# Optimization experiments

Hardware: AMD Instinct MI355X
Metric: run time of the kernel (lower is better)

## Reference

```python
import jax, jax.numpy as jnp
import numpy as np

N, IN, OUT, RANK = 8192, 4096, 4096, 256

def setup_inputs() -> dict:
    key = jax.random.key(0)
    ks = jax.random.split(key, 7)
    x = jax.random.normal(ks[0], (N, IN), dtype=jnp.float32)
    # original frozen linear layer params
    W = jax.random.normal(ks[1], (OUT, IN), dtype=jnp.float32) * (1.0 / np.sqrt(IN))
    bias = jax.random.normal(ks[2], (OUT,), dtype=jnp.float32) * 0.01
    # frozen shared low-rank matrices (kaiming-uniform-like scale)
    A_frozen = jax.random.normal(ks[3], (RANK, IN), dtype=jnp.float32) * (1.0 / np.sqrt(IN))
    B_frozen = jax.random.normal(ks[4], (OUT, RANK), dtype=jnp.float32) * (1.0 / np.sqrt(RANK))
    # trainable VeRA vectors (b_vec is zeros at init; use small randn so delta is nonzero)
    b_vec = jax.random.normal(ks[5], (OUT,), dtype=jnp.float32) * 0.01
    d_vec = jnp.full((RANK,), 0.1, dtype=jnp.float32) + jax.random.normal(ks[6], (RANK,), dtype=jnp.float32) * 0.01
    return {"x": x, "W": W, "bias": bias, "A_frozen": A_frozen, "B_frozen": B_frozen, "b_vec": b_vec, "d_vec": d_vec}

def reference(x, W, bias, A_frozen, B_frozen, b_vec, d_vec):
    # original frozen linear: [N, OUT]
    orig = x @ W.T + bias
    # diag(b) @ B @ diag(d) @ A @ x.T  ==  (((x @ A.T) * d) @ B.T) * b, transposed
    h = (x @ A_frozen.T) * d_vec            # [N, RANK]
    delta = (h @ B_frozen.T) * b_vec        # [N, OUT]
    return orig + delta
```

## Files before the change

kernel.cpp:

```cpp
#include <hip/hip_runtime.h>

#define IN_DIM 4096
#define OUT_DIM 4096
#define N_ROWS 8192
#define RANK 256

typedef __bf16 bf16x8 __attribute__((ext_vector_type(8)));
typedef float f32x4 __attribute__((ext_vector_type(4)));
typedef unsigned short u16;
typedef unsigned short u16x4 __attribute__((ext_vector_type(4)));

__device__ __forceinline__ u16 f2b(float f) {
    unsigned int u = __builtin_bit_cast(unsigned int, f);
    unsigned int r = u + 0x7FFFu + ((u >> 16) & 1u);
    return (u16)(r >> 16);
}

__device__ __forceinline__ void async16(const void* g, const void* l) {
    __builtin_amdgcn_global_load_lds(
        (const __attribute__((address_space(1))) void*)g,
        (__attribute__((address_space(3))) void*)l, 16, 0, 0);
}

__global__ __launch_bounds__(256) void cvt4(const float* __restrict__ s,
                                            u16* __restrict__ d, int n4) {
    int i = blockIdx.x * 256 + threadIdx.x;
    if (i >= n4) return;
    f32x4 v = __builtin_nontemporal_load((const f32x4*)s + i);
    u16x4 o;
    o.x = f2b(v.x); o.y = f2b(v.y); o.z = f2b(v.z); o.w = f2b(v.w);
    *((u16x4*)d + i) = o;
}

__global__ __launch_bounds__(256) void vera_adt(const float* __restrict__ A,
                                                const float* __restrict__ d,
                                                u16* __restrict__ adt) {
    int r = threadIdx.x;
    int i0 = blockIdx.x * 64;
    float dv = d[r];
    const float* ap = A + (size_t)r * IN_DIM + i0;
#pragma unroll 4
    for (int j = 0; j < 64; ++j)
        adt[(size_t)(i0 + j) * RANK + r] = f2b(__builtin_nontemporal_load(ap + j) * dv);
}

template <int MODE, int K, int NN, int TM, int TN>
__global__ __launch_bounds__(256) void vera_gemm(
    const u16* __restrict__ Aop, const u16* __restrict__ Bop,
    const float* __restrict__ W, const float* __restrict__ bvec,
    void* __restrict__ outv) {
    __shared__ __align__(16) __bf16 As[128 * 32];
    __shared__ __align__(16) __bf16 Bs[128 * 32];

    const int tid = threadIdx.x;
    const int lane = tid & 63;
    const int wavei = __builtin_amdgcn_readfirstlane(tid >> 6);
    const int fr = lane & 15;
    const int fq = lane >> 4;
    const int wm = (wavei >> 1) * 64;
    const int wn = (wavei & 1) * 64;

    constexpr int G = 8;
    const int bid = blockIdx.x;
    const int g = bid / (G * TN);
    const int r = bid - g * (G * TN);
    const int bm = (g * G + (r & (G - 1))) * 128;
    const int bn = (r / G) * 128;

    const int srow = tid >> 2;
    const int sk = (tid & 3) * 8;
    const u16* ga0 = Aop + (size_t)(bm + srow) * K + sk;
    const u16* ga1 = Aop + (size_t)(bm + 64 + srow) * K + sk;
    const u16* gb0 = Bop + (size_t)(bn + srow) * K + sk;
    const u16* gb1 = Bop + (size_t)(bn + 64 + srow) * K + sk;

    char* lAs = (char*)As;
    char* lBs = (char*)Bs;
    const int lo = wavei * 1024;

    f32x4 acc[4][4] = {};

    for (int k0 = 0; k0 < K; k0 += 32) {
        __syncthreads();
        async16(ga0 + k0, lAs + lo);
        async16(ga1 + k0, lAs + 4096 + lo);
        async16(gb0 + k0, lBs + lo);
        async16(gb1 + k0, lBs + 4096 + lo);
        __syncthreads();

        const __bf16* ap = As + (wm + fr) * 32 + fq * 8;
        const __bf16* bp = Bs + (wn + fr) * 32 + fq * 8;
        bf16x8 af[4], bfr[4];
#pragma unroll
        for (int i = 0; i < 4; ++i) {
            af[i] = *(const bf16x8*)(ap + i * 16 * 32);
            bfr[i] = *(const bf16x8*)(bp + i * 16 * 32);
        }
#pragma unroll
        for (int mi = 0; mi < 4; ++mi)
#pragma unroll
            for (int ni = 0; ni < 4; ++ni)
                acc[mi][ni] = __builtin_amdgcn_mfma_f32_16x16x32_bf16(
                    af[mi], bfr[ni], acc[mi][ni], 0, 0, 0);
    }

#pragma unroll
    for (int ni = 0; ni < 4; ++ni) {
        const int col = bn + wn + ni * 16 + fr;
        float bcol = (MODE == 1) ? bvec[col] : 0.f;
#pragma unroll
        for (int mi = 0; mi < 4; ++mi) {
            const int row0 = bm + wm + mi * 16 + fq * 4;
#pragma unroll
            for (int v = 0; v < 4; ++v) {
                const int row = row0 + v;
                float a = acc[mi][ni][v];
                if (MODE == 0) {
                    float wv = __builtin_nontemporal_load(&W[(size_t)row * NN + col]);
                    ((u16*)outv)[(size_t)row * NN + col] = f2b(wv + bvec[row] * a);
                } else {
                    __builtin_nontemporal_store(a + bcol,
                        &((float*)outv)[(size_t)row * NN + col]);
                }
            }
        }
    }
}

extern "C" void kernel_launch(void* const* d_in, const int* in_sizes, int n_in,
                              void* d_out, int out_size, void* d_ws, size_t ws_size,
                              hipStream_t stream) {
    (void)in_sizes; (void)n_in; (void)out_size; (void)ws_size;
    const float* x    = (const float*)d_in[0];
    const float* W    = (const float*)d_in[1];
    const float* bias = (const float*)d_in[2];
    const float* A    = (const float*)d_in[3];
    const float* B    = (const float*)d_in[4];
    const float* bv   = (const float*)d_in[5];
    const float* dv   = (const float*)d_in[6];

    char* ws = (char*)d_ws;
    u16* xb  = (u16*)ws;
    u16* wb  = (u16*)(ws + (size_t)N_ROWS * IN_DIM * 2);
    u16* adt = (u16*)(ws + (size_t)N_ROWS * IN_DIM * 2
                         + (size_t)OUT_DIM * IN_DIM * 2);
    u16* Bb  = adt + (size_t)IN_DIM * RANK;

    cvt4<<<dim3(OUT_DIM * RANK / 4 / 256), 256, 0, stream>>>(B, Bb, OUT_DIM * RANK / 4);
    vera_adt<<<dim3(IN_DIM / 64), 256, 0, stream>>>(A, dv, adt);
    vera_gemm<0, RANK, IN_DIM, OUT_DIM / 128, IN_DIM / 128>
        <<<dim3((OUT_DIM / 128) * (IN_DIM / 128)), 256, 0, stream>>>(
        Bb, adt, W, bv, wb);
    cvt4<<<dim3(N_ROWS * IN_DIM / 4 / 256), 256, 0, stream>>>(x, xb, N_ROWS * IN_DIM / 4);
    vera_gemm<1, IN_DIM, OUT_DIM, N_ROWS / 128, OUT_DIM / 128>
        <<<dim3((N_ROWS / 128) * (OUT_DIM / 128)), 256, 0, stream>>>(
        xb, wb, nullptr, bias, d_out);
}
```

Measured before the change: 608.9 us.

## Fuse prep kernels, overlap x conversion with weight GEMM, widen K step

Merges the B conversion and the A·diag(d) transpose into one prep kernel. The x fp32-to-bf16 conversion now runs in extra blocks appended to the weight-merging GEMM launch, so it overlaps with that GEMM. The main GEMM loads 64-wide K chunks per barrier pair instead of 32, which halves the number of sync rounds but doubles LDS use per block and may lower occupancy. Five launches become three.

```diff
diff --git a/kernel.cpp b/kernel.cpp
--- a/kernel.cpp
+++ b/kernel.cpp
@@ -22,37 +22,51 @@
         (__attribute__((address_space(3))) void*)l, 16, 0, 0);
 }
 
-__global__ __launch_bounds__(256) void cvt4(const float* __restrict__ s,
-                                            u16* __restrict__ d, int n4) {
-    int i = blockIdx.x * 256 + threadIdx.x;
-    if (i >= n4) return;
-    f32x4 v = __builtin_nontemporal_load((const f32x4*)s + i);
-    u16x4 o;
-    o.x = f2b(v.x); o.y = f2b(v.y); o.z = f2b(v.z); o.w = f2b(v.w);
-    *((u16x4*)d + i) = o;
+__global__ __launch_bounds__(256) void vera_prep(
+    const float* __restrict__ A, const float* __restrict__ dvec,
+    const float* __restrict__ B, u16* __restrict__ adt, u16* __restrict__ Bb) {
+    int b = blockIdx.x;
+    int t = threadIdx.x;
+    if (b < 128) {
+        int i0 = b * 32;
+        float dv = dvec[t];
+        const float* ap = A + (size_t)t * IN_DIM + i0;
+#pragma unroll 8
+        for (int j = 0; j < 32; ++j)
+            adt[(size_t)(i0 + j) * RANK + t] =
+                f2b(__builtin_nontemporal_load(ap + j) * dv);
+    } else {
+        int i = (b - 128) * 256 + t;
+        f32x4 v = __builtin_nontemporal_load((const f32x4*)B + i);
+        u16x4 o;
+        o.x = f2b(v.x); o.y = f2b(v.y); o.z = f2b(v.z); o.w = f2b(v.w);
+        *((u16x4*)Bb + i) = o;
+    }
 }
 
-__global__ __launch_bounds__(256) void vera_adt(const float* __restrict__ A,
-                                                const float* __restrict__ d,
-                                                u16* __restrict__ adt) {
-    int r = threadIdx.x;
-    int i0 = blockIdx.x * 64;
-    float dv = d[r];
-    const float* ap = A + (size_t)r * IN_DIM + i0;
-#pragma unroll 4
-    for (int j = 0; j < 64; ++j)
-        adt[(size_t)(i0 + j) * RANK + r] = f2b(__builtin_nontemporal_load(ap + j) * dv);
-}
-
-template <int MODE, int K, int NN, int TM, int TN>
+template <int MODE, int K, int NN, int TN, int GB>
 __global__ __launch_bounds__(256) void vera_gemm(
     const u16* __restrict__ Aop, const u16* __restrict__ Bop,
     const float* __restrict__ W, const float* __restrict__ bvec,
-    void* __restrict__ outv) {
-    __shared__ __align__(16) __bf16 As[128 * 32];
-    __shared__ __align__(16) __bf16 Bs[128 * 32];
+    void* __restrict__ outv,
+    const float* __restrict__ cvt_src, u16* __restrict__ cvt_dst, int cvt_n4) {
+    __shared__ __align__(16) __bf16 As[2 * 128 * 32];
+    __shared__ __align__(16) __bf16 Bs[2 * 128 * 32];
 
     const int tid = threadIdx.x;
+    const int bid = blockIdx.x;
+
+    if (bid >= GB) {
+        const int nb = gridDim.x - GB;
+        for (int i = (bid - GB) * 256 + tid; i < cvt_n4; i += nb * 256) {
+            f32x4 v = __builtin_nontemporal_load((const f32x4*)cvt_src + i);
+            u16x4 o;
+            o.x = f2b(v.x); o.y = f2b(v.y); o.z = f2b(v.z); o.w = f2b(v.w);
+            *((u16x4*)cvt_dst + i) = o;
+        }
+        return;
+    }
+
     const int lane = tid & 63;
     const int wavei = __builtin_amdgcn_readfirstlane(tid >> 6);
     const int fr = lane & 15;
@@ -60,12 +74,10 @@
     const int wm = (wavei >> 1) * 64;
     const int wn = (wavei & 1) * 64;
 
-    constexpr int G = 8;
-    const int bid = blockIdx.x;
-    const int g = bid / (G * TN);
-    const int r = bid - g * (G * TN);
-    const int bm = (g * G + (r & (G - 1))) * 128;
-    const int bn = (r / G) * 128;
+    const int g = bid / (8 * TN);
+    const int r = bid - g * (8 * TN);
+    const int bm = (g * 8 + (r & 7)) * 128;
+    const int bn = (r >> 3) * 128;
 
     const int srow = tid >> 2;
     const int sk = (tid & 3) * 8;
@@ -80,28 +92,35 @@
 
     f32x4 acc[4][4] = {};
 
-    for (int k0 = 0; k0 < K; k0 += 32) {
+    for (int k0 = 0; k0 < K; k0 += 64) {
         __syncthreads();
-        async16(ga0 + k0, lAs + lo);
-        async16(ga1 + k0, lAs + 4096 + lo);
-        async16(gb0 + k0, lBs + lo);
-        async16(gb1 + k0, lBs + 4096 + lo);
+        async16(ga0 + k0,      lAs + lo);
+        async16(ga1 + k0,      lAs + 4096 + lo);
+        async16(ga0 + k0 + 32, lAs + 8192 + lo);
+        async16(ga1 + k0 + 32, lAs + 12288 + lo);
+        async16(gb0 + k0,      lBs + lo);
+        async16(gb1 + k0,      lBs + 4096 + lo);
+        async16(gb0 + k0 + 32, lBs + 8192 + lo);
+        async16(gb1 + k0 + 32, lBs + 12288 + lo);
         __syncthreads();
 
-        const __bf16* ap = As + (wm + fr) * 32 + fq * 8;
-        const __bf16* bp = Bs + (wn + fr) * 32 + fq * 8;
-        bf16x8 af[4], bfr[4];
 #pragma unroll
-        for (int i = 0; i < 4; ++i) {
-            af[i] = *(const bf16x8*)(ap + i * 16 * 32);
-            bfr[i] = *(const bf16x8*)(bp + i * 16 * 32);
+        for (int ks = 0; ks < 2; ++ks) {
+            const __bf16* ap = As + ks * 4096 + (wm + fr) * 32 + fq * 8;
+            const __bf16* bp = Bs + ks * 4096 + (wn + fr) * 32 + fq * 8;
+            bf16x8 af[4], bfr[4];
+#pragma unroll
+            for (int i = 0; i < 4; ++i) {
+                af[i] = *(const bf16x8*)(ap + i * 16 * 32);
+                bfr[i] = *(const bf16x8*)(bp + i * 16 * 32);
+            }
+#pragma unroll
+            for (int mi = 0; mi < 4; ++mi)
+#pragma unroll
+                for (int ni = 0; ni < 4; ++ni)
+                    acc[mi][ni] = __builtin_amdgcn_mfma_f32_16x16x32_bf16(
+                        af[mi], bfr[ni], acc[mi][ni], 0, 0, 0);
         }
-#pragma unroll
-        for (int mi = 0; mi < 4; ++mi)
-#pragma unroll
-            for (int ni = 0; ni < 4; ++ni)
-                acc[mi][ni] = __builtin_amdgcn_mfma_f32_16x16x32_bf16(
-                    af[mi], bfr[ni], acc[mi][ni], 0, 0, 0);
     }
 
 #pragma unroll
@@ -146,13 +165,12 @@
                          + (size_t)OUT_DIM * IN_DIM * 2);
     u16* Bb  = adt + (size_t)IN_DIM * RANK;
 
-    cvt4<<<dim3(OUT_DIM * RANK / 4 / 256), 256, 0, stream>>>(B, Bb, OUT_DIM * RANK / 4);
-    vera_adt<<<dim3(IN_DIM / 64), 256, 0, stream>>>(A, dv, adt);
-    vera_gemm<0, RANK, IN_DIM, OUT_DIM / 128, IN_DIM / 128>
-        <<<dim3((OUT_DIM / 128) * (IN_DIM / 128)), 256, 0, stream>>>(
-        Bb, adt, W, bv, wb);
-    cvt4<<<dim3(N_ROWS * IN_DIM / 4 / 256), 256, 0, stream>>>(x, xb, N_ROWS * IN_DIM / 4);
-    vera_gemm<1, IN_DIM, OUT_DIM, N_ROWS / 128, OUT_DIM / 128>
-        <<<dim3((N_ROWS / 128) * (OUT_DIM / 128)), 256, 0, stream>>>(
-        xb, wb, nullptr, bias, d_out);
+    vera_prep<<<dim3(128 + OUT_DIM * RANK / 4 / 256), 256, 0, stream>>>(
+        A, dv, B, adt, Bb);
+    vera_gemm<0, RANK, IN_DIM, IN_DIM / 128, 1024>
+        <<<dim3(1024 + 2048), 256, 0, stream>>>(
+        Bb, adt, W, bv, wb, x, xb, N_ROWS * IN_DIM / 4);
+    vera_gemm<1, IN_DIM, OUT_DIM, OUT_DIM / 128, 2048>
+        <<<dim3(2048), 256, 0, stream>>>(
+        xb, wb, nullptr, bias, d_out, nullptr, nullptr, 0);
 }
```

After: 631.4 us. 3.7% more time.
